# Kernel optimization log

Hardware: AMD Instinct MI355X
Metric: run time of the kernel (lower is better)

## Reference

```python
import jax, jax.numpy as jnp
import numpy as np

N = 50000
E = 800000
NFEAT, NHID, NCLASS = 256, 128, 32


def setup_inputs() -> dict:
    key = jax.random.key(0)
    ks = jax.random.split(key, 8)
    x = jax.random.normal(ks[0], (N, NFEAT), dtype=jnp.float32)
    edge_src = jax.random.randint(ks[1], (E,), 0, N, dtype=jnp.int32)
    edge_dst = jax.random.randint(ks[2], (E,), 0, N, dtype=jnp.int32)
    edge_weight = jax.random.uniform(ks[3], (E,), dtype=jnp.float32)
    # Linear layer params (torch Linear: y = x @ W.T + b); store as [in, out]
    s1 = 1.0 / np.sqrt(NFEAT)
    s2 = 1.0 / np.sqrt(NHID)
    W1 = jax.random.uniform(ks[4], (NFEAT, NHID), jnp.float32, -s1, s1)
    b1 = jax.random.uniform(ks[5], (NHID,), jnp.float32, -s1, s1)
    W2 = jax.random.uniform(ks[6], (NHID, NCLASS), jnp.float32, -s2, s2)
    b2 = jax.random.uniform(ks[7], (NCLASS,), jnp.float32, -s2, s2)
    return {"x": x, "edge_src": edge_src, "edge_dst": edge_dst,
            "edge_weight": edge_weight, "W1": W1, "b1": b1, "W2": W2, "b2": b2}


def spmm(edge_src, edge_dst, edge_weight, h):
    # out[dst] += w * h[src]  -- sparse adjacency @ dense features
    msgs = edge_weight[:, None] * h[edge_src]          # [E, F]
    return jax.ops.segment_sum(msgs, edge_dst, num_segments=N)


def reference(x, edge_src, edge_dst, edge_weight, W1, b1, W2, b2):
    # GCN layer 1: Linear -> SpMM -> ReLU (dropout inactive in eval mode)
    h = x @ W1 + b1                                    # [N, NHID]
    h = spmm(edge_src, edge_dst, edge_weight, h)
    h = jax.nn.relu(h)
    # GCN layer 2: Linear -> SpMM
    h = h @ W2 + b2                                    # [N, NCLASS]
    out = spmm(edge_src, edge_dst, edge_weight, h)
    return out
```

## Files before the change

### kernel.cpp

```cpp
#include <hip/hip_runtime.h>

#define NFEAT 256
#define NHID 128
#define NCLASS 32

typedef __attribute__((ext_vector_type(8))) short short8;
typedef __attribute__((ext_vector_type(4))) float f32x4;
typedef __attribute__((ext_vector_type(4))) int int4v;

static __device__ __forceinline__ unsigned short f2bf(float f) {
    unsigned u = __float_as_uint(f);
    unsigned r = (u + 0x7fffu + ((u >> 16) & 1u)) >> 16;
    return (unsigned short)r;
}
static __device__ __forceinline__ float bf_lo(unsigned d) {
    return __uint_as_float(d << 16);
}
static __device__ __forceinline__ float bf_hi(unsigned d) {
    return __uint_as_float(d & 0xffff0000u);
}

__global__ __launch_bounds__(256) void prep_kernel(
    const float* __restrict__ W1, unsigned short* __restrict__ W1t,
    const float* __restrict__ W2, float4* __restrict__ w2t4,
    const int* __restrict__ dst, int* __restrict__ bkt_counts, int E, int shift)
{
    const int tid = threadIdx.x;
    if (blockIdx.x < 128) {
        int o = blockIdx.x * 256 + tid;
        int c = o >> 8, k = o & 255;
        W1t[o] = f2bf(W1[(size_t)k * NHID + c]);
    } else if (blockIdx.x == 128) {
#pragma unroll
        for (int j = 0; j < 4; ++j) {
            int o = tid + j * 256;
            int c = o >> 5, sp = o & 31;
            int s = sp ^ (c & 7);
            float4 v;
            v.x = W2[(size_t)(s * 4 + 0) * NCLASS + c];
            v.y = W2[(size_t)(s * 4 + 1) * NCLASS + c];
            v.z = W2[(size_t)(s * 4 + 2) * NCLASS + c];
            v.w = W2[(size_t)(s * 4 + 3) * NCLASS + c];
            w2t4[o] = v;
        }
    } else {
        __shared__ int h[256];
        const int kb = blockIdx.x - 129;
        h[tid] = 0;
        __syncthreads();
        for (int e = kb * 256 + tid; e < E; e += 256 * 256)
            atomicAdd(&h[dst[e] >> shift], 1);
        __syncthreads();
        int v = h[tid];
        if (v) atomicAdd(&bkt_counts[tid], v);
    }
}

__global__ __launch_bounds__(256) void gemm1_mfma_kernel(
    const float* __restrict__ x, const unsigned short* __restrict__ W1t,
    const float* __restrict__ b1, unsigned short* __restrict__ h1b, int N)
{
    __shared__ unsigned short wt[128 * 256];
    __shared__ unsigned short xs[64 * 64];

    const int tid = threadIdx.x;
    const int lane = tid & 63;
    const int wv = tid >> 6;
    const int row0 = blockIdx.x * 64;
    const int l15 = lane & 15;
    const int l47 = lane >> 4;
    const int r7 = lane & 7;

    {
        const int4v* src = (const int4v*)W1t;
#pragma unroll
        for (int j = 0; j < 16; ++j) {
            int si = tid + j * 256;
            int c = si >> 5, s = si & 31;
            int sp = (s & 24) | ((s & 7) ^ (c & 7));
            int4v v = src[si];
            *(int4v*)&wt[c * 256 + sp * 8] = v;
        }
    }

    auto stage_x = [&](int t) {
#pragma unroll
        for (int j = 0; j < 2; ++j) {
            int si = tid + j * 256;
            int r = si >> 3, s = si & 7;
            int row = row0 + r;
            float4 v0 = make_float4(0.f, 0.f, 0.f, 0.f), v1 = v0;
            if (row < N) {
                const float4* xp = (const float4*)&x[(size_t)row * NFEAT + t * 64 + s * 8];
                v0 = xp[0]; v1 = xp[1];
            }
            int w0 = f2bf(v0.x) | ((unsigned)f2bf(v0.y) << 16);
            int w1 = f2bf(v0.z) | ((unsigned)f2bf(v0.w) << 16);
            int w2 = f2bf(v1.x) | ((unsigned)f2bf(v1.y) << 16);
            int w3 = f2bf(v1.z) | ((unsigned)f2bf(v1.w) << 16);
            int sp = s ^ (r & 7);
            int4v pv; pv[0] = w0; pv[1] = w1; pv[2] = w2; pv[3] = w3;
            *(int4v*)&xs[r * 64 + sp * 8] = pv;
        }
    };

    f32x4 acc[8];
#pragma unroll
    for (int cf = 0; cf < 8; ++cf)
#pragma unroll
        for (int r = 0; r < 4; ++r) acc[cf][r] = 0.f;

    stage_x(0);
    __syncthreads();

    const int arow = wv * 16 + l15;
#pragma unroll
    for (int t = 0; t < 4; ++t) {
        short8 af[2];
#pragma unroll
        for (int kf = 0; kf < 2; ++kf) {
            int slot = (kf * 4 + l47) ^ r7;
            af[kf] = *(const short8*)&xs[arow * 64 + slot * 8];
        }
#pragma unroll
        for (int cf = 0; cf < 8; ++cf) {
            const int brow = cf * 16 + l15;
#pragma unroll
            for (int kf = 0; kf < 2; ++kf) {
                int slot = t * 8 + ((kf * 4 + l47) ^ r7);
                short8 bfr = *(const short8*)&wt[brow * 256 + slot * 8];
                acc[cf] = __builtin_amdgcn_mfma_f32_16x16x32_bf16(af[kf], bfr, acc[cf], 0, 0, 0);
            }
        }
        __syncthreads();
        if (t < 3) {
            stage_x(t + 1);
            __syncthreads();
        }
    }

#pragma unroll
    for (int cf = 0; cf < 8; ++cf) {
        float bias = b1[cf * 16 + l15];
#pragma unroll
        for (int r = 0; r < 4; ++r) {
            int row = row0 + wv * 16 + l47 * 4 + r;
            if (row < N)
                h1b[(size_t)row * NHID + cf * 16 + l15] = f2bf(acc[cf][r] + bias);
        }
    }
}

__global__ __launch_bounds__(256) void bucket_scan_kernel(
    const int* __restrict__ bkt_counts, int* __restrict__ bkt_base,
    int* __restrict__ bkt_cursor)
{
    __shared__ int s[256];
    const int t = threadIdx.x;
    int v = bkt_counts[t];
    s[t] = v;
    __syncthreads();
    for (int off = 1; off < 256; off <<= 1) {
        int tv = (t >= off) ? s[t - off] : 0;
        __syncthreads();
        s[t] += tv;
        __syncthreads();
    }
    int excl = s[t] - v;
    bkt_base[t] = excl;
    bkt_cursor[t] = excl;
    if (t == 255) bkt_base[256] = s[255];
}

#define SC_EPT 8
__global__ __launch_bounds__(256) void bucket_scatter_kernel(
    const int* __restrict__ src, const int* __restrict__ dst,
    const float* __restrict__ w, int* __restrict__ bkt_cursor,
    uint2* __restrict__ bkt_edges, int E, int shift)
{
    __shared__ int h[256];
    __shared__ int base[256];
    const int tid = threadIdx.x;
    const int e0 = blockIdx.x * (256 * SC_EPT);
    h[tid] = 0;
    __syncthreads();
#pragma unroll
    for (int j = 0; j < SC_EPT; ++j) {
        int e = e0 + tid + j * 256;
        if (e < E) atomicAdd(&h[dst[e] >> shift], 1);
    }
    __syncthreads();
    int c = h[tid];
    base[tid] = c ? atomicAdd(&bkt_cursor[tid], c) : 0;
    __syncthreads();
    h[tid] = 0;
    __syncthreads();
#pragma unroll
    for (int j = 0; j < SC_EPT; ++j) {
        int e = e0 + tid + j * 256;
        if (e < E) {
            int d = dst[e];
            int b = d >> shift;
            int lp = atomicAdd(&h[b], 1);
            uint2 rec;
            rec.x = (unsigned)src[e] | ((unsigned)(d & ((1 << shift) - 1)) << 24);
            rec.y = __float_as_uint(w[e]);
            bkt_edges[base[b] + lp] = rec;
        }
    }
}

__global__ __launch_bounds__(1024) void fine_scatter_kernel(
    const int* __restrict__ bkt_base, const uint2* __restrict__ bkt_edges,
    int* __restrict__ row_ptr, uint2* __restrict__ csr_e,
    int shift, int N, int E)
{
    __shared__ int h[256];
    __shared__ int cur[256];
    const int b = blockIdx.x;
    const int t = threadIdx.x;
    const int lo = bkt_base[b], hi = bkt_base[b + 1];
    const int dbase = b << shift;

    if (t < 256) h[t] = 0;
    __syncthreads();
    for (int i = lo + t; i < hi; i += 1024)
        atomicAdd(&h[bkt_edges[i].x >> 24], 1);
    __syncthreads();
    int v = (t < 256) ? h[t] : 0;
    for (int off = 1; off < 256; off <<= 1) {
        int tv = (t >= off && t < 256) ? h[t - off] : 0;
        __syncthreads();
        if (t < 256) h[t] += tv;
        __syncthreads();
    }
    if (t < 256) {
        int excl = h[t] - v;
        int r = dbase + t;
        if (r < N) row_ptr[r] = lo + excl;
        cur[t] = lo + excl;
    }
    if (b == 0 && t == 0) row_ptr[N] = E;
    __syncthreads();
    for (int i = lo + t; i < hi; i += 1024) {
        uint2 rec = bkt_edges[i];
        int dl = rec.x >> 24;
        int pos = atomicAdd(&cur[dl], 1);
        uint2 o;
        o.x = rec.x & 0xFFFFFFu;
        o.y = rec.y;
        csr_e[pos] = o;
    }
}

__global__ __launch_bounds__(512) void spmm1_gemm2_kernel(
    const int* __restrict__ row_ptr, const uint2* __restrict__ csr_e,
    const unsigned short* __restrict__ h1b, const float4* __restrict__ w2t4,
    const float* __restrict__ b2, unsigned* __restrict__ h2b, int N)
{
    __shared__ float4 w2s4[32 * 32];
    __shared__ float hrow[8][NHID];
    const int tid = threadIdx.x;
#pragma unroll
    for (int j = 0; j < 2; ++j) {
        int idx = tid + j * 512;
        w2s4[idx] = w2t4[idx];
    }
    __syncthreads();

    const int lane = tid & 63;
    const int wv = tid >> 6;
    const int row = __builtin_amdgcn_readfirstlane(blockIdx.x * 8 + wv);
    if (row >= N) return;

    const int e0 = row_ptr[row], e1 = row_ptr[row + 1];
    const size_t loff = (size_t)(lane * 2);
    float a0 = 0.f, a1 = 0.f;
    int e = e0;
    for (; e + 8 <= e1; e += 8) {
        uint2 r[8];
#pragma unroll
        for (int j = 0; j < 8; ++j) r[j] = csr_e[e + j];
        unsigned d[8];
#pragma unroll
        for (int j = 0; j < 8; ++j)
            d[j] = *(const unsigned*)(h1b + (size_t)r[j].x * NHID + loff);
#pragma unroll
        for (int j = 0; j < 8; ++j) {
            float w = __uint_as_float(r[j].y);
            a0 += w * bf_lo(d[j]); a1 += w * bf_hi(d[j]);
        }
    }
    for (; e + 2 <= e1; e += 2) {
        uint2 r0 = csr_e[e], r1 = csr_e[e + 1];
        unsigned d0 = *(const unsigned*)(h1b + (size_t)r0.x * NHID + loff);
        unsigned d1 = *(const unsigned*)(h1b + (size_t)r1.x * NHID + loff);
        float w0 = __uint_as_float(r0.y), w1 = __uint_as_float(r1.y);
        a0 += w0 * bf_lo(d0); a1 += w0 * bf_hi(d0);
        a0 += w1 * bf_lo(d1); a1 += w1 * bf_hi(d1);
    }
    if (e < e1) {
        uint2 r = csr_e[e];
        float w = __uint_as_float(r.y);
        unsigned d = *(const unsigned*)(h1b + (size_t)r.x * NHID + loff);
        a0 += w * bf_lo(d); a1 += w * bf_hi(d);
    }
    *(float2*)&hrow[wv][lane * 2] = make_float2(fmaxf(a0, 0.f), fmaxf(a1, 0.f));

    const int c = lane & 31;
    const int half = lane >> 5;
    const float4* hb = (const float4*)&hrow[wv][half * 64];
    const int cs7 = c & 7;
    float acc = 0.f;
#pragma unroll
    for (int k4 = 0; k4 < 16; ++k4) {
        int s = half * 16 + k4;
        float4 w4 = w2s4[c * 32 + (s ^ cs7)];
        float4 h4 = hb[k4];
        acc += h4.x * w4.x + h4.y * w4.y + h4.z * w4.z + h4.w * w4.w;
    }
    acc += __shfl(acc, lane ^ 32);
    float accb = acc + b2[c];
    float nb = __shfl(accb, lane ^ 1);
    if (half == 0 && (lane & 1) == 0) {
        unsigned u = (unsigned)f2bf(accb) | ((unsigned)f2bf(nb) << 16);
        h2b[(size_t)row * 16 + (lane >> 1)] = u;
    }
}

__global__ __launch_bounds__(256) void spmm2_kernel(
    const int* __restrict__ row_ptr, const uint2* __restrict__ csr_e,
    const unsigned* __restrict__ h2b, float* __restrict__ out, int N)
{
    const int li = threadIdx.x & 15;
    const int g = threadIdx.x >> 4;
    const int row = blockIdx.x * 16 + g;
    if (row >= N) return;
    const int e0 = row_ptr[row], e1 = row_ptr[row + 1];
    float a0 = 0.f, a1 = 0.f;
    int e = e0;
    for (; e + 8 <= e1; e += 8) {
        uint2 r[8];
#pragma unroll
        for (int j = 0; j < 8; ++j) r[j] = csr_e[e + j];
        unsigned d[8];
#pragma unroll
        for (int j = 0; j < 8; ++j) d[j] = h2b[(size_t)r[j].x * 16 + li];
#pragma unroll
        for (int j = 0; j < 8; ++j) {
            float w = __uint_as_float(r[j].y);
            a0 += w * bf_lo(d[j]); a1 += w * bf_hi(d[j]);
        }
    }
    for (; e + 2 <= e1; e += 2) {
        uint2 r0 = csr_e[e], r1 = csr_e[e + 1];
        unsigned d0 = h2b[(size_t)r0.x * 16 + li];
        unsigned d1 = h2b[(size_t)r1.x * 16 + li];
        float w0 = __uint_as_float(r0.y), w1 = __uint_as_float(r1.y);
        a0 += w0 * bf_lo(d0); a1 += w0 * bf_hi(d0);
        a0 += w1 * bf_lo(d1); a1 += w1 * bf_hi(d1);
    }
    if (e < e1) {
        uint2 r = csr_e[e];
        float w = __uint_as_float(r.y);
        unsigned d = h2b[(size_t)r.x * 16 + li];
        a0 += w * bf_lo(d); a1 += w * bf_hi(d);
    }
    *(float2*)&out[(size_t)row * NCLASS + li * 2] = make_float2(a0, a1);
}


extern "C" void kernel_launch(void* const* d_in, const int* in_sizes, int n_in,
                              void* d_out, int out_size, void* d_ws, size_t ws_size,
                              hipStream_t stream) {
    const float* x    = (const float*)d_in[0];
    const int*   esrc = (const int*)d_in[1];
    const int*   edst = (const int*)d_in[2];
    const float* ew   = (const float*)d_in[3];
    const float* W1   = (const float*)d_in[4];
    const float* b1   = (const float*)d_in[5];
    const float* W2   = (const float*)d_in[6];
    const float* b2   = (const float*)d_in[7];
    float* out = (float*)d_out;

    const int N = in_sizes[0] / NFEAT;
    const int E = in_sizes[1];

    int shift = 0;
    while (((N - 1) >> shift) >= 256) ++shift;
    const int NBKT = ((N - 1) >> shift) + 1;

    char* base = (char*)d_ws;
    size_t off = 0;
    auto take = [&](size_t bytes) -> void* {
        void* p = base + off;
        off += (bytes + 255) & ~(size_t)255;
        return p;
    };
    unsigned short* h1b = (unsigned short*)take((size_t)N * NHID * sizeof(unsigned short));
    unsigned* h2b  = (unsigned*)take((size_t)N * 16 * sizeof(unsigned));
    int*   row_ptr = (int*)take((size_t)(N + 1) * sizeof(int));
    int*   bkt_counts  = (int*)take(256 * sizeof(int));
    int*   bkt_base    = (int*)take(257 * sizeof(int));
    int*   bkt_cursor  = (int*)take(256 * sizeof(int));
    uint2* bkt_edges   = (uint2*)take((size_t)E * sizeof(uint2));
    uint2* csr_e       = (uint2*)take((size_t)E * sizeof(uint2));
    unsigned short* W1t = (unsigned short*)take((size_t)NFEAT * NHID * sizeof(unsigned short));
    float4* w2t4       = (float4*)take(1024 * sizeof(float4));
    (void)ws_size; (void)n_in; (void)out_size;

    hipMemsetAsync(bkt_counts, 0, 256 * sizeof(int), stream);
    prep_kernel<<<385, 256, 0, stream>>>(W1, W1t, W2, w2t4, edst, bkt_counts, E, shift);
    gemm1_mfma_kernel<<<(N + 63) / 64, 256, 0, stream>>>(x, W1t, b1, h1b, N);
    bucket_scan_kernel<<<1, 256, 0, stream>>>(bkt_counts, bkt_base, bkt_cursor);
    bucket_scatter_kernel<<<(E + 256 * SC_EPT - 1) / (256 * SC_EPT), 256, 0, stream>>>(
        esrc, edst, ew, bkt_cursor, bkt_edges, E, shift);
    fine_scatter_kernel<<<NBKT, 1024, 0, stream>>>(bkt_base, bkt_edges, row_ptr, csr_e,
                                                   shift, N, E);
    spmm1_gemm2_kernel<<<(N + 7) / 8, 512, 0, stream>>>(row_ptr, csr_e, h1b, w2t4, b2, h2b, N);
    spmm2_kernel<<<(N + 15) / 16, 256, 0, stream>>>(row_ptr, csr_e, h2b, out, N);
}
```

Baseline: 119.8 us.

## Split each row's edges across two wavefronts in fused SpMM1+GEMM2 kernel

Doubles the block to 1024 threads so two wavefronts share each destination row, each summing half of the row's edges. The second half's partial sum goes through shared memory and is merged before the ReLU and the small W2 projection. The pre-transposed, swizzled W2 buffer is dropped; W2 is now loaded raw into LDS and read with scalar strided accesses. The aim is more memory-level parallelism per row for the gather-bound SpMM, at the cost of a block-wide barrier, a larger LDS footprint and less vectorised W2 reads.

```diff
diff --git a/kernel.cpp b/kernel.cpp
--- a/kernel.cpp
+++ b/kernel.cpp
@@ -22,7 +22,6 @@
 
 __global__ __launch_bounds__(256) void prep_kernel(
     const float* __restrict__ W1, unsigned short* __restrict__ W1t,
-    const float* __restrict__ W2, float4* __restrict__ w2t4,
     const int* __restrict__ dst, int* __restrict__ bkt_counts, int E, int shift)
 {
     const int tid = threadIdx.x;
@@ -30,22 +29,9 @@
         int o = blockIdx.x * 256 + tid;
         int c = o >> 8, k = o & 255;
         W1t[o] = f2bf(W1[(size_t)k * NHID + c]);
-    } else if (blockIdx.x == 128) {
-#pragma unroll
-        for (int j = 0; j < 4; ++j) {
-            int o = tid + j * 256;
-            int c = o >> 5, sp = o & 31;
-            int s = sp ^ (c & 7);
-            float4 v;
-            v.x = W2[(size_t)(s * 4 + 0) * NCLASS + c];
-            v.y = W2[(size_t)(s * 4 + 1) * NCLASS + c];
-            v.z = W2[(size_t)(s * 4 + 2) * NCLASS + c];
-            v.w = W2[(size_t)(s * 4 + 3) * NCLASS + c];
-            w2t4[o] = v;
-        }
     } else {
         __shared__ int h[256];
-        const int kb = blockIdx.x - 129;
+        const int kb = blockIdx.x - 128;
         h[tid] = 0;
         __syncthreads();
         for (int e = kb * 256 + tid; e < E; e += 256 * 256)
@@ -253,31 +239,38 @@
     }
 }
 
-__global__ __launch_bounds__(512) void spmm1_gemm2_kernel(
+__global__ __launch_bounds__(1024) void spmm1_gemm2_kernel(
     const int* __restrict__ row_ptr, const uint2* __restrict__ csr_e,
-    const unsigned short* __restrict__ h1b, const float4* __restrict__ w2t4,
+    const unsigned short* __restrict__ h1b, const float* __restrict__ W2,
     const float* __restrict__ b2, unsigned* __restrict__ h2b, int N)
 {
-    __shared__ float4 w2s4[32 * 32];
+    __shared__ float w2s[NHID * NCLASS];
     __shared__ float hrow[8][NHID];
+    __shared__ float hpart[8][NHID];
     const int tid = threadIdx.x;
 #pragma unroll
-    for (int j = 0; j < 2; ++j) {
-        int idx = tid + j * 512;
-        w2s4[idx] = w2t4[idx];
+    for (int j = 0; j < 4; ++j) {
+        int idx = tid + j * 1024;
+        w2s[idx] = W2[idx];
     }
     __syncthreads();
 
     const int lane = tid & 63;
     const int wv = tid >> 6;
-    const int row = __builtin_amdgcn_readfirstlane(blockIdx.x * 8 + wv);
-    if (row >= N) return;
-
-    const int e0 = row_ptr[row], e1 = row_ptr[row + 1];
+    const int rloc = wv & 7;
+    const int half = wv >> 3;
+    const int row = __builtin_amdgcn_readfirstlane(blockIdx.x * 8 + rloc);
+
+    int e0 = 0, e1 = 0;
+    if (row < N) { e0 = row_ptr[row]; e1 = row_ptr[row + 1]; }
+    const int mid = e0 + ((e1 - e0) >> 1);
+    const int es = half ? mid : e0;
+    const int et = half ? e1 : mid;
+
     const size_t loff = (size_t)(lane * 2);
     float a0 = 0.f, a1 = 0.f;
-    int e = e0;
-    for (; e + 8 <= e1; e += 8) {
+    int e = es;
+    for (; e + 8 <= et; e += 8) {
         uint2 r[8];
 #pragma unroll
         for (int j = 0; j < 8; ++j) r[j] = csr_e[e + j];
@@ -291,38 +284,61 @@
             a0 += w * bf_lo(d[j]); a1 += w * bf_hi(d[j]);
         }
     }
-    for (; e + 2 <= e1; e += 2) {
+    if (e + 4 <= et) {
+        uint2 r[4];
+#pragma unroll
+        for (int j = 0; j < 4; ++j) r[j] = csr_e[e + j];
+        unsigned d[4];
+#pragma unroll
+        for (int j = 0; j < 4; ++j)
+            d[j] = *(const unsigned*)(h1b + (size_t)r[j].x * NHID + loff);
+#pragma unroll
+        for (int j = 0; j < 4; ++j) {
+            float w = __uint_as_float(r[j].y);
+            a0 += w * bf_lo(d[j]); a1 += w * bf_hi(d[j]);
+        }
+        e += 4;
+    }
+    if (e + 2 <= et) {
         uint2 r0 = csr_e[e], r1 = csr_e[e + 1];
         unsigned d0 = *(const unsigned*)(h1b + (size_t)r0.x * NHID + loff);
         unsigned d1 = *(const unsigned*)(h1b + (size_t)r1.x * NHID + loff);
         float w0 = __uint_as_float(r0.y), w1 = __uint_as_float(r1.y);
         a0 += w0 * bf_lo(d0); a1 += w0 * bf_hi(d0);
         a0 += w1 * bf_lo(d1); a1 += w1 * bf_hi(d1);
-    }
-    if (e < e1) {
+        e += 2;
+    }
+    if (e < et) {
         uint2 r = csr_e[e];
         float w = __uint_as_float(r.y);
         unsigned d = *(const unsigned*)(h1b + (size_t)r.x * NHID + loff);
         a0 += w * bf_lo(d); a1 += w * bf_hi(d);
     }
-    *(float2*)&hrow[wv][lane * 2] = make_float2(fmaxf(a0, 0.f), fmaxf(a1, 0.f));
+
+    if (half)
+        *(float2*)&hpart[rloc][lane * 2] = make_float2(a0, a1);
+    __syncthreads();
+    if (half) return;
+
+    {
+        float2 p = *(const float2*)&hpart[rloc][lane * 2];
+        a0 = fmaxf(a0 + p.x, 0.f);
+        a1 = fmaxf(a1 + p.y, 0.f);
+        *(float2*)&hrow[rloc][lane * 2] = make_float2(a0, a1);
+    }
 
     const int c = lane & 31;
-    const int half = lane >> 5;
-    const float4* hb = (const float4*)&hrow[wv][half * 64];
-    const int cs7 = c & 7;
+    const int kh = lane >> 5;
+    const float* hw = &hrow[rloc][kh * 64];
+    const float* wp = &w2s[(size_t)kh * 64 * NCLASS + c];
     float acc = 0.f;
 #pragma unroll
-    for (int k4 = 0; k4 < 16; ++k4) {
-        int s = half * 16 + k4;
-        float4 w4 = w2s4[c * 32 + (s ^ cs7)];
-        float4 h4 = hb[k4];
-        acc += h4.x * w4.x + h4.y * w4.y + h4.z * w4.z + h4.w * w4.w;
-    }
+    for (int k = 0; k < 64; ++k)
+        acc += hw[k] * wp[k * NCLASS];
     acc += __shfl(acc, lane ^ 32);
     float accb = acc + b2[c];
     float nb = __shfl(accb, lane ^ 1);
-    if (half == 0 && (lane & 1) == 0) {
+    if (kh == 0 && (lane & 1) == 0 && row < N) {
         unsigned u = (unsigned)f2bf(accb) | ((unsigned)f2bf(nb) << 16);
         h2b[(size_t)row * 16 + (lane >> 1)] = u;
     }
@@ -406,17 +422,16 @@
     uint2* bkt_edges   = (uint2*)take((size_t)E * sizeof(uint2));
     uint2* csr_e       = (uint2*)take((size_t)E * sizeof(uint2));
     unsigned short* W1t = (unsigned short*)take((size_t)NFEAT * NHID * sizeof(unsigned short));
-    float4* w2t4       = (float4*)take(1024 * sizeof(float4));
     (void)ws_size; (void)n_in; (void)out_size;
 
     hipMemsetAsync(bkt_counts, 0, 256 * sizeof(int), stream);
-    prep_kernel<<<385, 256, 0, stream>>>(W1, W1t, W2, w2t4, edst, bkt_counts, E, shift);
+    prep_kernel<<<384, 256, 0, stream>>>(W1, W1t, edst, bkt_counts, E, shift);
     gemm1_mfma_kernel<<<(N + 63) / 64, 256, 0, stream>>>(x, W1t, b1, h1b, N);
     bucket_scan_kernel<<<1, 256, 0, stream>>>(bkt_counts, bkt_base, bkt_cursor);
     bucket_scatter_kernel<<<(E + 256 * SC_EPT - 1) / (256 * SC_EPT), 256, 0, stream>>>(
         esrc, edst, ew, bkt_cursor, bkt_edges, E, shift);
     fine_scatter_kernel<<<NBKT, 1024, 0, stream>>>(bkt_base, bkt_edges, row_ptr, csr_e,
                                                    shift, N, E);
-    spmm1_gemm2_kernel<<<(N + 7) / 8, 512, 0, stream>>>(row_ptr, csr_e, h1b, w2t4, b2, h2b, N);
+    spmm1_gemm2_kernel<<<(N + 7) / 8, 1024, 0, stream>>>(row_ptr, csr_e, h1b, W2, b2, h2b, N);
     spmm2_kernel<<<(N + 15) / 16, 256, 0, stream>>>(row_ptr, csr_e, h2b, out, N);
 }
```

After: 140.7 us. +17.4%, slower.
